# Kernel optimization log

Hardware: AMD Instinct MI355X
Metric: run time of the kernel (lower is better)

Reference implementation:

```python
import jax, jax.numpy as jnp
import numpy as np
from itertools import permutations

NEG = -1e30  # finite 'log-zero' sentinel to keep grads NaN-free
DEN_SCALE = 1.0


def fsm_log_marginal(llh, seqlen, src, dst, pdf, weight, init, final):
    """Log-marginal (total log path weight) of an FSM over a sequence.

    llh: [T, C] frame pdf log-likelihoods; arcs (src,dst,pdf,weight): [A];
    init/final: [N] state log-weights. Forward recursion:
      alpha_{t+1}[j] = logsumexp_{arcs a: dst=j} alpha_t[src_a] + w_a + llh[t, pdf_a]
    Frames t >= seqlen are identity (alpha frozen).
    """
    N = init.shape[0]
    T = llh.shape[0]

    def step(alpha, xs):
        llh_t, t = xs
        score = alpha[src] + weight + llh_t[pdf]  # [A]
        m = jnp.maximum(jax.ops.segment_max(score, dst, num_segments=N), NEG)
        s = jax.ops.segment_sum(jnp.exp(score - m[dst]), dst, num_segments=N)
        new = m + jnp.log(jnp.maximum(s, 1e-30))
        alpha = jnp.where(t < seqlen, new, alpha)
        return alpha, None

    alpha, _ = jax.lax.scan(step, init, (llh, jnp.arange(T)))
    return jax.nn.logsumexp(alpha + final)


# vmap over batch (FSM shared -> None axes) for the denominator
_den_b = jax.vmap(fsm_log_marginal, in_axes=(0, 0, None, None, None, None, None, None))
_den_sb = jax.vmap(_den_b, in_axes=(0, 0, None, None, None, None, None, None))
# vmap over (speaker, batch) with per-(s,b) numerator FSMs
_num_sb = jax.vmap(jax.vmap(fsm_log_marginal))


def reference(est_llhs, seqlengths, den_src, den_dst, den_pdf, den_weight,
              den_init, den_final, num_src, num_dst, num_pdf, num_weight,
              num_init, num_final):
    S = est_llhs.shape[1]
    llhs = jnp.transpose(est_llhs, (1, 0, 2, 3))  # [S, B, T, C]
    seql = seqlengths.T                           # [S, B]

    # denominator: shared graph, summed over speakers -> [B]
    den = _den_sb(llhs, seql, den_src, den_dst, den_pdf, den_weight,
                  den_init, den_final)  # [S, B]
    den_llh = den.sum(axis=0)

    # numerator: evaluate every speaker permutation, take min over perms
    num_per_perm = []
    for p in permutations(range(S)):
        pidx = jnp.array(p)
        nl = _num_sb(llhs[pidx], seql[pidx], num_src, num_dst, num_pdf,
                     num_weight, num_init, num_final)  # [S, B]
        num_per_perm.append(nl.sum(axis=0))
    num_llh = jnp.min(jnp.stack(num_per_perm, axis=1), axis=1)  # [B]

    loss = -(num_llh - DEN_SCALE * den_llh)
    return loss.sum()


def setup_inputs() -> dict:
    key = jax.random.key(0)
    ks = jax.random.split(key, 14)
    B, S, T, C = 8, 2, 512, 2048
    Nd, Ad = 1024, 16384   # denominator graph
    Nn, An = 256, 2048     # numerator graphs (per speaker, per utt)

    est_llhs = jax.nn.log_softmax(
        jax.random.normal(ks[0], (B, S, T, C), jnp.float32), axis=-1)
    seqlengths = jax.random.randint(ks[1], (B, S), T // 2, T + 1, jnp.int32)

    den_src = jax.random.randint(ks[2], (Ad,), 0, Nd, jnp.int32)
    den_dst = jax.random.randint(ks[3], (Ad,), 0, Nd, jnp.int32)
    den_pdf = jax.random.randint(ks[4], (Ad,), 0, C, jnp.int32)
    den_weight = 0.1 * jax.random.normal(ks[5], (Ad,), jnp.float32)
    den_init = jax.nn.log_softmax(jax.random.normal(ks[6], (Nd,), jnp.float32))
    den_final = jax.nn.log_softmax(jax.random.normal(ks[7], (Nd,), jnp.float32))

    num_src = jax.random.randint(ks[8], (S, B, An), 0, Nn, jnp.int32)
    num_dst = jax.random.randint(ks[9], (S, B, An), 0, Nn, jnp.int32)
    num_pdf = jax.random.randint(ks[10], (S, B, An), 0, C, jnp.int32)
    num_weight = 0.1 * jax.random.normal(ks[11], (S, B, An), jnp.float32)
    num_init = jax.nn.log_softmax(
        jax.random.normal(ks[12], (S, B, Nn), jnp.float32), axis=-1)
    num_final = jax.nn.log_softmax(
        jax.random.normal(ks[13], (S, B, Nn), jnp.float32), axis=-1)

    return {
        'est_llhs': est_llhs, 'seqlengths': seqlengths,
        'den_src': den_src, 'den_dst': den_dst, 'den_pdf': den_pdf,
        'den_weight': den_weight, 'den_init': den_init, 'den_final': den_final,
        'num_src': num_src, 'num_dst': num_dst, 'num_pdf': num_pdf,
        'num_weight': num_weight, 'num_init': num_init, 'num_final': num_final,
    }
```

## Files before the change

kernel.cpp:

```cpp
#include <hip/hip_runtime.h>
#include <cstdint>
#include <cstddef>

#define BB 8
#define SS 2
#define TT 512
#define CC 2048
#define ND 1024
#define AD 16384
#define NN 256
#define AN 2048
#define NEGV -1e30f
#define NTH 1024

__global__ void prep_kernel(const int* __restrict__ src, const int* __restrict__ dst,
                            const int* __restrict__ pdf, const float* __restrict__ w,
                            unsigned* __restrict__ meta_t, float* __restrict__ w_t,
                            unsigned* __restrict__ pxi,
                            int* __restrict__ pbeg, int* __restrict__ padj,
                            int N, int A, int LC)
{
    __shared__ int cnt[1024];
    __shared__ int pos[1024];
    const int g = blockIdx.x;
    src += (size_t)g * A; dst += (size_t)g * A; pdf += (size_t)g * A; w += (size_t)g * A;
    meta_t += (size_t)g * A; w_t += (size_t)g * A; pxi += (size_t)g * A;
    pbeg += (size_t)g * (N + 1); padj += (size_t)g * N;
    const int tid = threadIdx.x;
    cnt[tid] = 0;
    __syncthreads();
    for (int a = tid; a < A; a += blockDim.x) atomicAdd(&cnt[dst[a]], 1);
    __syncthreads();
    const int deg = cnt[tid];
    pos[tid] = deg;
    __syncthreads();
    for (int off = 1; off < blockDim.x; off <<= 1) {
        int add = (tid >= off) ? pos[tid - off] : 0;
        __syncthreads();
        pos[tid] += add;
        __syncthreads();
    }
    const int r0 = pos[tid] - deg;
    const int np = deg ? (((r0 + deg - 1) >> LC) - (r0 >> LC) + 1) : 0;
    __syncthreads();
    pos[tid] = np;
    __syncthreads();
    for (int off = 1; off < blockDim.x; off <<= 1) {
        int add = (tid >= off) ? pos[tid - off] : 0;
        __syncthreads();
        pos[tid] += add;
        __syncthreads();
    }
    const int pexcl = pos[tid] - np;
    pbeg[tid] = pexcl;
    if (tid == blockDim.x - 1) pbeg[N] = pexcl + np;
    padj[tid] = pexcl - (r0 >> LC);
    cnt[tid] = r0;
    __syncthreads();
    for (int a = tid; a < A; a += blockDim.x) {
        const int d2 = dst[a];
        const int p = atomicAdd(&cnt[d2], 1);
        const int l = p >> LC;
        const int i = p & ((1 << LC) - 1);
        meta_t[(size_t)i * NTH + l] =
            (unsigned)src[a] | ((unsigned)pdf[a] << 10) | ((unsigned)d2 << 21);
        w_t[(size_t)i * NTH + l] = w[a];
        pxi[p] = (unsigned)pdf[a];
    }
}

__global__ __launch_bounds__(256) void wprep_kernel(
    const float* __restrict__ est,
    const unsigned* __restrict__ pxi_den, const unsigned* __restrict__ pxi_num,
    float* __restrict__ Wd, float* __restrict__ Wn, int t0, int Tt)
{
    __shared__ float row_s[CC];
    const int tid = threadIdx.x;
    int bid = blockIdx.x;
    if (bid < 16 * Tt) {
        const int q = bid & 15, trel = bid >> 4;
        const int t = t0 + trel;
        const int s = q >> 3, b = q & 7;
        const float* row = est + ((size_t)(b * SS + s) * TT + t) * CC;
        for (int k = tid; k < CC; k += 256) row_s[k] = row[k];
        __syncthreads();
        float4* out = (float4*)(Wd + (size_t)(trel * 16 + q) * (16 * 1024));
        const uint4* p4 = (const uint4*)pxi_den;
        for (int k = 0; k < 16; ++k) {
            const int o4 = k * 256 + tid;
            const uint4 pp = p4[o4];
            out[o4] = make_float4(row_s[pp.x], row_s[pp.y], row_s[pp.z], row_s[pp.w]);
        }
    } else {
        bid -= 16 * Tt;
        const int r = bid & 31, trel = bid >> 5;
        const int t = t0 + trel;
        const int g = r & 15, p = r >> 4;
        const int s = g >> 3, b = g & 7;
        const int sp = p ? (1 - s) : s;
        const float* row = est + ((size_t)(b * SS + sp) * TT + t) * CC;
        for (int k = tid; k < CC; k += 256) row_s[k] = row[k];
        __syncthreads();
        float4* out = (float4*)(Wn + (size_t)(trel * 32 + r) * (2 * 1024));
        const uint4* p4 = (const uint4*)(pxi_num + (size_t)g * AN);
        for (int k = 0; k < 2; ++k) {
            const int o4 = k * 256 + tid;
            const uint4 pp = p4[o4];
            out[o4] = make_float4(row_s[pp.x], row_s[pp.y], row_s[pp.z], row_s[pp.w]);
        }
    }
}

template<int CH>
__device__ inline void load_w_row(const float* __restrict__ p, float* dst)
{
    if constexpr (CH == 16) {
        const float4* p4 = (const float4*)p;
        const float4 a = p4[0], b = p4[1], c = p4[2], d = p4[3];
        dst[0]=a.x;  dst[1]=a.y;  dst[2]=a.z;  dst[3]=a.w;
        dst[4]=b.x;  dst[5]=b.y;  dst[6]=b.z;  dst[7]=b.w;
        dst[8]=c.x;  dst[9]=c.y;  dst[10]=c.z; dst[11]=c.w;
        dst[12]=d.x; dst[13]=d.y; dst[14]=d.z; dst[15]=d.w;
    } else {
        const float2 v = *(const float2*)p;
        dst[0] = v.x; dst[1] = v.y;
    }
}

template<int CH>
__device__ void fsm_forward_tile(int N, int L, int t0, int Tt, bool first, bool last,
    const float* __restrict__ Wrow0, int wstride,
    const unsigned* __restrict__ meta_g, const float* __restrict__ w_g,
    const int* __restrict__ pbeg_g, const int* __restrict__ padj_g,
    const float* __restrict__ initv, const float* __restrict__ finalv,
    float* __restrict__ alpha_gl, float* __restrict__ res,
    float* alpha_s, float2* pk)
{
    const int tid = threadIdx.x;
    unsigned meta[CH]; float wreg[CH];
#pragma unroll
    for (int i = 0; i < CH; ++i) {
        meta[i] = meta_g[i * NTH + tid];
        wreg[i] = w_g[i * NTH + tid];
    }
    unsigned segmask = 0;
#pragma unroll
    for (int i = 0; i < CH; ++i) {
        const int di = (int)(meta[i] >> 21);
        const int dn = (i + 1 < CH) ? (int)(meta[i + 1] >> 21) : -1;
        if (di != dn) segmask |= (1u << i);
    }
    const int slot0 = padj_g[meta[0] >> 21] + tid;
    const bool st = tid < N;
    int pb0 = 0, pb1 = 0; float fin = 0.f;
    if (st) {
        alpha_s[tid] = first ? initv[tid] : alpha_gl[tid];
        pb0 = pbeg_g[tid]; pb1 = pbeg_g[tid + 1];
        fin = finalv[tid];
    }
    int tb = L - t0; if (tb > Tt) tb = Tt; if (tb < 0) tb = 0;
    float wc[CH];
    if (tb > 0) load_w_row<CH>(Wrow0 + (size_t)tid * CH, wc);
    __syncthreads();

    constexpr int G = (CH < 8) ? CH : 8;
    for (int trel = 0; trel < tb; ++trel) {
        const bool pre = (trel + 1 < tb);
        float wn[CH];
        if (pre)
            load_w_row<CH>(Wrow0 + (size_t)(trel + 1) * wstride + (size_t)tid * CH, wn);
        float m = -INFINITY, ss = 0.f;
        int sl = slot0;
#pragma unroll
        for (int i0 = 0; i0 < CH; i0 += G) {
            float av[G];
#pragma unroll
            for (int gi = 0; gi < G; ++gi)
                av[gi] = alpha_s[meta[i0 + gi] & 1023u];
#pragma unroll
            for (int gi = 0; gi < G; ++gi) {
                const float sc = (av[gi] + wreg[i0 + gi]) + wc[i0 + gi];
                const float d = sc - m;
                const float e = __expf(-fabsf(d));
                if (d > 0.f) { ss = ss * e + 1.f; m = sc; }
                else         { ss += e; }
                if (segmask & (1u << (i0 + gi))) {
                    pk[sl] = make_float2(m, ss); ++sl;
                    m = -INFINITY; ss = 0.f;
                }
            }
        }
        __syncthreads();
        if (st) {
            float mm, s2;
            const int cnt = pb1 - pb0;
            if (cnt > 0) {
                const float2 P0 = pk[pb0];
                const float2 P1 = pk[cnt > 1 ? pb0 + 1 : pb0];
                const float2 P2 = pk[cnt > 2 ? pb0 + 2 : pb0];
                const float2 P3 = pk[cnt > 3 ? pb0 + 3 : pb0];
                mm = P0.x; s2 = P0.y;
                if (cnt > 1) {
                    const float d = P1.x - mm; const float e = __expf(-fabsf(d));
                    if (d > 0.f) { s2 = s2 * e + P1.y; mm = P1.x; } else { s2 += P1.y * e; }
                }
                if (cnt > 2) {
                    const float d = P2.x - mm; const float e = __expf(-fabsf(d));
                    if (d > 0.f) { s2 = s2 * e + P2.y; mm = P2.x; } else { s2 += P2.y * e; }
                }
                if (cnt > 3) {
                    const float d = P3.x - mm; const float e = __expf(-fabsf(d));
                    if (d > 0.f) { s2 = s2 * e + P3.y; mm = P3.x; } else { s2 += P3.y * e; }
                }
                for (int q2 = pb0 + 4; q2 < pb1; ++q2) {
                    const float2 Pq = pk[q2];
                    const float d = Pq.x - mm; const float e = __expf(-fabsf(d));
                    if (d > 0.f) { s2 = s2 * e + Pq.y; mm = Pq.x; } else { s2 += Pq.y * e; }
                }
                const float mc  = fmaxf(mm, NEGV);
                const float scs = s2 * __expf(mm - mc);
                alpha_s[tid] = mc + __logf(fmaxf(scs, 1e-30f));
            } else {
                alpha_s[tid] = NEGV + __logf(1e-30f);
            }
        }
        __syncthreads();
        if (pre) {
#pragma unroll
            for (int i = 0; i < CH; ++i) wc[i] = wn[i];
        }
    }

    if (last) {
        const float v = st ? (alpha_s[tid] + fin) : -INFINITY;
        float* red = (float*)pk;
        red[tid] = v;
        __syncthreads();
        for (int off = 512; off > 0; off >>= 1) {
            if (tid < off) red[tid] = fmaxf(red[tid], red[tid + off]);
            __syncthreads();
        }
        const float M = red[0];
        __syncthreads();
        red[tid] = __expf(v - M);
        __syncthreads();
        for (int off = 512; off > 0; off >>= 1) {
            if (tid < off) red[tid] += red[tid + off];
            __syncthreads();
        }
        if (tid == 0) *res = M + __logf(red[0]);
    } else if (st) {
        alpha_gl[tid] = alpha_s[tid];
    }
}

__global__ __launch_bounds__(1024) void fwd_kernel(
    const int* __restrict__ seqlen,
    const float* __restrict__ Wd, const float* __restrict__ Wn,
    const unsigned* __restrict__ den_meta, const float* __restrict__ den_w,
    const int* __restrict__ den_pbeg, const int* __restrict__ den_padj,
    const float* __restrict__ den_init, const float* __restrict__ den_final,
    const unsigned* __restrict__ num_meta, const float* __restrict__ num_w,
    const int* __restrict__ num_pbeg, const int* __restrict__ num_padj,
    const float* __restrict__ num_init, const float* __restrict__ num_final,
    float* __restrict__ alpha_g, float* __restrict__ res,
    int t0, int Tt, int last)
{
    __shared__ float alpha[1024];
    __shared__ float2 pk[2048];
    const int bid = blockIdx.x;
    const bool first = (t0 == 0);
    if (bid < 16) {
        const int s = bid >> 3, b = bid & 7;
        const int L = seqlen[b * SS + s];
        fsm_forward_tile<16>(ND, L, t0, Tt, first, last != 0,
                             Wd + (size_t)bid * (16 * 1024), 16 * 16 * 1024,
                             den_meta, den_w, den_pbeg, den_padj,
                             den_init, den_final,
                             alpha_g + (size_t)bid * 1024, &res[bid], alpha, pk);
    } else {
        const int q = bid - 16;
        const int p = q >> 4, g = q & 15;
        const int s = g >> 3, b = g & 7;
        const int sp = p ? (1 - s) : s;
        const int L = seqlen[b * SS + sp];
        fsm_forward_tile<2>(NN, L, t0, Tt, first, last != 0,
                            Wn + (size_t)q * (2 * 1024), 32 * 2 * 1024,
                            num_meta + (size_t)g * AN, num_w + (size_t)g * AN,
                            num_pbeg + (size_t)g * (NN + 1), num_padj + (size_t)g * NN,
                            num_init + (size_t)g * NN, num_final + (size_t)g * NN,
                            alpha_g + (size_t)bid * 1024, &res[16 + q], alpha, pk);
    }
}

__global__ void finalize_kernel(const float* __restrict__ res, float* __restrict__ out)
{
    if (threadIdx.x == 0 && blockIdx.x == 0) {
        float loss = 0.f;
        for (int b = 0; b < BB; ++b) {
            const float den = res[b] + res[8 + b];
            const float n0  = res[16 + b] + res[16 + 8 + b];
            const float n1  = res[32 + b] + res[32 + 8 + b];
            const float nm  = fminf(n0, n1);
            loss += -(nm - den);
        }
        out[0] = loss;
    }
}

extern "C" void kernel_launch(void* const* d_in, const int* in_sizes, int n_in,
                              void* d_out, int out_size, void* d_ws, size_t ws_size,
                              hipStream_t stream)
{
    const float* est       = (const float*)d_in[0];
    const int*   seqlen    = (const int*)  d_in[1];
    const int*   den_src   = (const int*)  d_in[2];
    const int*   den_dst   = (const int*)  d_in[3];
    const int*   den_pdf   = (const int*)  d_in[4];
    const float* den_w     = (const float*)d_in[5];
    const float* den_init  = (const float*)d_in[6];
    const float* den_final = (const float*)d_in[7];
    const int*   num_src   = (const int*)  d_in[8];
    const int*   num_dst   = (const int*)  d_in[9];
    const int*   num_pdf   = (const int*)  d_in[10];
    const float* num_w     = (const float*)d_in[11];
    const float* num_init  = (const float*)d_in[12];
    const float* num_final = (const float*)d_in[13];

    char* ws = (char*)d_ws;
    unsigned* den_meta = (unsigned*)(ws + 0);
    float*    den_wt   = (float*)   (ws + 65536);
    unsigned* num_meta = (unsigned*)(ws + 131072);
    float*    num_wt   = (float*)   (ws + 262144);
    unsigned* den_pxi  = (unsigned*)(ws + 393216);
    unsigned* num_pxi  = (unsigned*)(ws + 458752);
    int*      den_pbeg = (int*)     (ws + 589824);
    int*      num_pbeg = (int*)     (ws + 594176);
    int*      den_padj = (int*)     (ws + 610816);
    int*      num_padj = (int*)     (ws + 614912);
    float*    alpha_g  = (float*)   (ws + 631296);
    float*    res      = (float*)   (ws + 827904);
    const size_t fixed = 828416;

    int Tt = 64;
    while (Tt > 4 && fixed + (size_t)Tt * 1310720u > ws_size) Tt >>= 1;
    float* Wd = (float*)(ws + fixed);
    float* Wn = Wd + (size_t)Tt * 16 * 16384;

    prep_kernel<<<1, 1024, 0, stream>>>(den_src, den_dst, den_pdf, den_w,
                                        den_meta, den_wt, den_pxi,
                                        den_pbeg, den_padj, ND, AD, 4);
    prep_kernel<<<16, 256, 0, stream>>>(num_src, num_dst, num_pdf, num_w,
                                        num_meta, num_wt, num_pxi,
                                        num_pbeg, num_padj, NN, AN, 1);

    const int nt = TT / Tt;
    for (int k = 0; k < nt; ++k) {
        wprep_kernel<<<48 * Tt, 256, 0, stream>>>(est, den_pxi, num_pxi,
                                                  Wd, Wn, k * Tt, Tt);
        fwd_kernel<<<48, 1024, 0, stream>>>(seqlen, Wd, Wn,
                                            den_meta, den_wt, den_pbeg, den_padj,
                                            den_init, den_final,
                                            num_meta, num_wt, num_pbeg, num_padj,
                                            num_init, num_final,
                                            alpha_g, res, k * Tt, Tt,
                                            (k == nt - 1) ? 1 : 0);
    }

    finalize_kernel<<<1, 64, 0, stream>>>(res, (float*)d_out);
}
```

Before: 1.515 ms.

## Fuse next-tile weight gather into forward kernel and duplicate alpha to spread LDS banks

The separate per-tile gather kernel is replaced by a double-buffered scheme. The 32 numerator blocks, which finish quickly, gather emission weights for the next time tile while the denominator blocks run the forward recursion, which removes one kernel launch and its serialization per tile. Alpha is also written twice in shared memory, once as an XOR-swizzled copy, and prep greedily assigns each arc's source read to whichever copy has the less-loaded bank in its wavefront, to cut LDS bank conflicts. This doubles the weight workspace and adds shared memory per block, and gather throughput now depends on only 32 blocks.

```diff
diff --git a/kernel.cpp b/kernel.cpp
--- a/kernel.cpp
+++ b/kernel.cpp
@@ -22,6 +22,7 @@
 {
     __shared__ int cnt[1024];
     __shared__ int pos[1024];
+    __shared__ unsigned char gcnt[8192];
     const int g = blockIdx.x;
     src += (size_t)g * A; dst += (size_t)g * A; pdf += (size_t)g * A; w += (size_t)g * A;
     meta_t += (size_t)g * A; w_t += (size_t)g * A; pxi += (size_t)g * A;
@@ -62,53 +63,81 @@
         const int p = atomicAdd(&cnt[d2], 1);
         const int l = p >> LC;
         const int i = p & ((1 << LC) - 1);
-        meta_t[(size_t)i * NTH + l] =
-            (unsigned)src[a] | ((unsigned)pdf[a] << 10) | ((unsigned)d2 << 21);
+        meta_t[(size_t)i * NTH + l] = (unsigned)src[a] | ((unsigned)d2 << 16);
         w_t[(size_t)i * NTH + l] = w[a];
         pxi[p] = (unsigned)pdf[a];
     }
-}
-
-__global__ __launch_bounds__(256) void wprep_kernel(
+    __syncthreads();
+    const int CH = 1 << LC;
+    const int ngrp = (NTH / 64) * CH;
+    if (tid < ngrp) {
+        unsigned char* cb = &gcnt[tid * 32];
+        for (int b = 0; b < 32; ++b) cb[b] = 0;
+        const int i = tid & (CH - 1);
+        const int w2 = tid >> LC;
+        for (int lane = 0; lane < 64; ++lane) {
+            const size_t idx = (size_t)i * NTH + (w2 * 64 + lane);
+            const unsigned mt = meta_t[idx];
+            const unsigned sv = mt & 0xffffu;
+            const unsigned alt = sv ^ ((sv >> 5) & 31u);
+            const int b0 = (int)(sv & 31u), b1 = (int)(alt & 31u);
+            unsigned gx;
+            if (cb[b1] < cb[b0]) { cb[b1]++; gx = (unsigned)N + alt; }
+            else                 { cb[b0]++; gx = sv; }
+            meta_t[idx] = (mt & 0xffff0000u) | gx;
+        }
+    }
+}
+
+__device__ void wprep_part(int ub, int nb, int t0, int Tt, const float* __restrict__ est,
+                           const unsigned* __restrict__ pxi_den,
+                           const unsigned* __restrict__ pxi_num,
+                           float* __restrict__ Wd, float* __restrict__ Wn,
+                           float* row_s)
+{
+    const int tid = threadIdx.x;
+    const int nden = 16 * Tt;
+    const int total = nden + 32 * Tt;
+    for (int u = ub; u < total; u += nb) {
+        __syncthreads();
+        const float* row; const unsigned* pxi; float* out; int nar;
+        if (u < nden) {
+            const int inst = u / Tt, trel = u - inst * Tt;
+            const int s = inst >> 3, b = inst & 7;
+            row = est + ((size_t)(b * SS + s) * TT + (t0 + trel)) * CC;
+            pxi = pxi_den;
+            out = Wd + ((size_t)inst * Tt + trel) * AD;
+            nar = AD;
+        } else {
+            const int v = u - nden;
+            const int inst = v / Tt, trel = v - inst * Tt;
+            const int gg = inst & 15, p = inst >> 4;
+            const int s = gg >> 3, b = gg & 7;
+            const int sp = p ? (1 - s) : s;
+            row = est + ((size_t)(b * SS + sp) * TT + (t0 + trel)) * CC;
+            pxi = pxi_num + (size_t)gg * AN;
+            out = Wn + ((size_t)inst * Tt + trel) * AN;
+            nar = AN;
+        }
+        row_s[tid] = row[tid]; row_s[tid + 1024] = row[tid + 1024];
+        __syncthreads();
+        const uint4* p4 = (const uint4*)pxi;
+        float4* o4 = (float4*)out;
+        const int n4 = nar >> 2;
+        for (int k = tid; k < n4; k += 1024) {
+            const uint4 pp = p4[k];
+            o4[k] = make_float4(row_s[pp.x], row_s[pp.y], row_s[pp.z], row_s[pp.w]);
+        }
+    }
+}
+
+__global__ __launch_bounds__(1024) void wprep0_kernel(
     const float* __restrict__ est,
     const unsigned* __restrict__ pxi_den, const unsigned* __restrict__ pxi_num,
     float* __restrict__ Wd, float* __restrict__ Wn, int t0, int Tt)
 {
     __shared__ float row_s[CC];
-    const int tid = threadIdx.x;
-    int bid = blockIdx.x;
-    if (bid < 16 * Tt) {
-        const int q = bid & 15, trel = bid >> 4;
-        const int t = t0 + trel;
-        const int s = q >> 3, b = q & 7;
-        const float* row = est + ((size_t)(b * SS + s) * TT + t) * CC;
-        for (int k = tid; k < CC; k += 256) row_s[k] = row[k];
-        __syncthreads();
-        float4* out = (float4*)(Wd + (size_t)(trel * 16 + q) * (16 * 1024));
-        const uint4* p4 = (const uint4*)pxi_den;
-        for (int k = 0; k < 16; ++k) {
-            const int o4 = k * 256 + tid;
-            const uint4 pp = p4[o4];
-            out[o4] = make_float4(row_s[pp.x], row_s[pp.y], row_s[pp.z], row_s[pp.w]);
-        }
-    } else {
-        bid -= 16 * Tt;
-        const int r = bid & 31, trel = bid >> 5;
-        const int t = t0 + trel;
-        const int g = r & 15, p = r >> 4;
-        const int s = g >> 3, b = g & 7;
-        const int sp = p ? (1 - s) : s;
-        const float* row = est + ((size_t)(b * SS + sp) * TT + t) * CC;
-        for (int k = tid; k < CC; k += 256) row_s[k] = row[k];
-        __syncthreads();
-        float4* out = (float4*)(Wn + (size_t)(trel * 32 + r) * (2 * 1024));
-        const uint4* p4 = (const uint4*)(pxi_num + (size_t)g * AN);
-        for (int k = 0; k < 2; ++k) {
-            const int o4 = k * 256 + tid;
-            const uint4 pp = p4[o4];
-            out[o4] = make_float4(row_s[pp.x], row_s[pp.y], row_s[pp.z], row_s[pp.w]);
-        }
-    }
+    wprep_part(blockIdx.x, gridDim.x, t0, Tt, est, pxi_den, pxi_num, Wd, Wn, row_s);
 }
 
 template<int CH>
@@ -146,15 +175,17 @@
     unsigned segmask = 0;
 #pragma unroll
     for (int i = 0; i < CH; ++i) {
-        const int di = (int)(meta[i] >> 21);
-        const int dn = (i + 1 < CH) ? (int)(meta[i + 1] >> 21) : -1;
+        const int di = (int)(meta[i] >> 16);
+        const int dn = (i + 1 < CH) ? (int)(meta[i + 1] >> 16) : -1;
         if (di != dn) segmask |= (1u << i);
     }
-    const int slot0 = padj_g[meta[0] >> 21] + tid;
+    const int slot0 = padj_g[meta[0] >> 16] + tid;
     const bool st = tid < N;
     int pb0 = 0, pb1 = 0; float fin = 0.f;
     if (st) {
-        alpha_s[tid] = first ? initv[tid] : alpha_gl[tid];
+        const float a0 = first ? initv[tid] : alpha_gl[tid];
+        alpha_s[tid] = a0;
+        alpha_s[N + (tid ^ ((tid >> 5) & 31))] = a0;
         pb0 = pbeg_g[tid]; pb1 = pbeg_g[tid + 1];
         fin = finalv[tid];
     }
@@ -176,7 +207,7 @@
             float av[G];
 #pragma unroll
             for (int gi = 0; gi < G; ++gi)
-                av[gi] = alpha_s[meta[i0 + gi] & 1023u];
+                av[gi] = alpha_s[meta[i0 + gi] & 0xffffu];
 #pragma unroll
             for (int gi = 0; gi < G; ++gi) {
                 const float sc = (av[gi] + wreg[i0 + gi]) + wc[i0 + gi];
@@ -192,14 +223,14 @@
         }
         __syncthreads();
         if (st) {
-            float mm, s2;
+            float v2;
             const int cnt = pb1 - pb0;
             if (cnt > 0) {
                 const float2 P0 = pk[pb0];
                 const float2 P1 = pk[cnt > 1 ? pb0 + 1 : pb0];
                 const float2 P2 = pk[cnt > 2 ? pb0 + 2 : pb0];
                 const float2 P3 = pk[cnt > 3 ? pb0 + 3 : pb0];
-                mm = P0.x; s2 = P0.y;
+                float mm = P0.x, s2 = P0.y;
                 if (cnt > 1) {
                     const float d = P1.x - mm; const float e = __expf(-fabsf(d));
                     if (d > 0.f) { s2 = s2 * e + P1.y; mm = P1.x; } else { s2 += P1.y * e; }
@@ -219,10 +250,12 @@
                 }
                 const float mc  = fmaxf(mm, NEGV);
                 const float scs = s2 * __expf(mm - mc);
-                alpha_s[tid] = mc + __logf(fmaxf(scs, 1e-30f));
+                v2 = mc + __logf(fmaxf(scs, 1e-30f));
             } else {
-                alpha_s[tid] = NEGV + __logf(1e-30f);
+                v2 = NEGV + __logf(1e-30f);
             }
+            alpha_s[tid] = v2;
+            alpha_s[N + (tid ^ ((tid >> 5) & 31))] = v2;
         }
         __syncthreads();
         if (pre) {
@@ -254,7 +287,7 @@
     }
 }
 
-__global__ __launch_bounds__(1024) void fwd_kernel(
+__global__ __launch_bounds__(1024) void fused_kernel(
     const int* __restrict__ seqlen,
     const float* __restrict__ Wd, const float* __restrict__ Wn,
     const unsigned* __restrict__ den_meta, const float* __restrict__ den_w,
@@ -264,17 +297,21 @@
     const int* __restrict__ num_pbeg, const int* __restrict__ num_padj,
     const float* __restrict__ num_init, const float* __restrict__ num_final,
     float* __restrict__ alpha_g, float* __restrict__ res,
-    int t0, int Tt, int last)
-{
-    __shared__ float alpha[1024];
+    int t0, int Tt, int last,
+    const float* __restrict__ est,
+    const unsigned* __restrict__ pxi_den, const unsigned* __restrict__ pxi_num,
+    float* __restrict__ Wd_next, float* __restrict__ Wn_next)
+{
+    __shared__ float alpha[2048];
     __shared__ float2 pk[2048];
+    __shared__ float row_s[CC];
     const int bid = blockIdx.x;
     const bool first = (t0 == 0);
     if (bid < 16) {
         const int s = bid >> 3, b = bid & 7;
         const int L = seqlen[b * SS + s];
         fsm_forward_tile<16>(ND, L, t0, Tt, first, last != 0,
-                             Wd + (size_t)bid * (16 * 1024), 16 * 16 * 1024,
+                             Wd + (size_t)bid * Tt * AD, AD,
                              den_meta, den_w, den_pbeg, den_padj,
                              den_init, den_final,
                              alpha_g + (size_t)bid * 1024, &res[bid], alpha, pk);
@@ -285,11 +322,14 @@
         const int sp = p ? (1 - s) : s;
         const int L = seqlen[b * SS + sp];
         fsm_forward_tile<2>(NN, L, t0, Tt, first, last != 0,
-                            Wn + (size_t)q * (2 * 1024), 32 * 2 * 1024,
+                            Wn + (size_t)q * Tt * AN, AN,
                             num_meta + (size_t)g * AN, num_w + (size_t)g * AN,
                             num_pbeg + (size_t)g * (NN + 1), num_padj + (size_t)g * NN,
                             num_init + (size_t)g * NN, num_final + (size_t)g * NN,
                             alpha_g + (size_t)bid * 1024, &res[16 + q], alpha, pk);
+        if (!last)
+            wprep_part(q, 32, t0 + Tt, Tt, est, pxi_den, pxi_num,
+                       Wd_next, Wn_next, row_s);
     }
 }
 
@@ -343,9 +383,12 @@
     const size_t fixed = 828416;
 
     int Tt = 64;
-    while (Tt > 4 && fixed + (size_t)Tt * 1310720u > ws_size) Tt >>= 1;
-    float* Wd = (float*)(ws + fixed);
-    float* Wn = Wd + (size_t)Tt * 16 * 16384;
+    while (Tt > 4 && fixed + 2ull * (size_t)Tt * 1310720ull > ws_size) Tt >>= 1;
+    const size_t wbuf_f = (size_t)Tt * (16 * AD + 32 * AN);
+    float* Wd0 = (float*)(ws + fixed);
+    float* Wn0 = Wd0 + (size_t)16 * Tt * AD;
+    float* Wd1 = Wd0 + wbuf_f;
+    float* Wn1 = Wd1 + (size_t)16 * Tt * AD;
 
     prep_kernel<<<1, 1024, 0, stream>>>(den_src, den_dst, den_pdf, den_w,
                                         den_meta, den_wt, den_pxi,
@@ -354,17 +397,22 @@
                                         num_meta, num_wt, num_pxi,
                                         num_pbeg, num_padj, NN, AN, 1);
 
+    wprep0_kernel<<<256, 1024, 0, stream>>>(est, den_pxi, num_pxi, Wd0, Wn0, 0, Tt);
+
     const int nt = TT / Tt;
     for (int k = 0; k < nt; ++k) {
-        wprep_kernel<<<48 * Tt, 256, 0, stream>>>(est, den_pxi, num_pxi,
-                                                  Wd, Wn, k * Tt, Tt);
-        fwd_kernel<<<48, 1024, 0, stream>>>(seqlen, Wd, Wn,
-                                            den_meta, den_wt, den_pbeg, den_padj,
-                                            den_init, den_final,
-                                            num_meta, num_wt, num_pbeg, num_padj,
-                                            num_init, num_final,
-                                            alpha_g, res, k * Tt, Tt,
-                                            (k == nt - 1) ? 1 : 0);
+        float* WdC = (k & 1) ? Wd1 : Wd0;
+        float* WnC = (k & 1) ? Wn1 : Wn0;
+        float* WdN = (k & 1) ? Wd0 : Wd1;
+        float* WnN = (k & 1) ? Wn0 : Wn1;
+        fused_kernel<<<48, 1024, 0, stream>>>(seqlen, WdC, WnC,
+                                              den_meta, den_wt, den_pbeg, den_padj,
+                                              den_init, den_final,
+                                              num_meta, num_wt, num_pbeg, num_padj,
+                                              num_init, num_final,
+                                              alpha_g, res, k * Tt, Tt,
+                                              (k == nt - 1) ? 1 : 0,
+                                              est, den_pxi, num_pxi, WdN, WnN);
     }
 
     finalize_kernel<<<1, 64, 0, stream>>>(res, (float*)d_out);
```

New measurement: 1.627 ms. 7.4% more time.
